# Optimization experiments

Measured on AMD Instinct MI355X. Metric: run time of the kernel, lower is better.

Reference implementation:

```python
import jax, jax.numpy as jnp
import numpy as np

EPS = 1e-05
DELTA = 2.0


def setup_inputs() -> dict:
    key = jax.random.key(0)
    k1, k2, k3, k4 = jax.random.split(key, 4)
    b, n, d = 8, 2048, 256
    static_node_emb = jax.random.normal(k1, (n, d), dtype=jnp.float32)
    current_node_emb = jax.random.normal(k2, (b, n, d), dtype=jnp.float32)
    prev_node_emb = jax.random.normal(k3, (b, n, d), dtype=jnp.float32)
    # xavier_normal for (d, 1): std = sqrt(2/(d+1))
    threshold_pool = jax.random.normal(k4, (d, 1), dtype=jnp.float32) * np.sqrt(2.0 / (d + 1))
    gamma = jnp.ones((1,), dtype=jnp.float32)
    beta = jnp.zeros((1,), dtype=jnp.float32)
    return {
        'static_node_emb': static_node_emb,
        'current_node_emb': current_node_emb,
        'prev_node_emb': prev_node_emb,
        'threshold_pool': threshold_pool,
        'gamma': gamma,
        'beta': beta,
    }


def reference(static_node_emb, current_node_emb, prev_node_emb, threshold_pool, gamma, beta):
    # graph: [b, n, n]
    graph = jnp.einsum('bnd,bmd->bnm', current_node_emb, prev_node_emb)
    # static mask: relu(S S^T) > 0  -> {0,1} float [n, n]
    static_sim = jnp.einsum('nd,md->nm', static_node_emb, static_node_emb)
    static_mask = (jax.nn.relu(static_sim) > 0).astype(jnp.float32)
    # masked relu + row-normalize (asym_adj)
    masked = jax.nn.relu(graph * static_mask) + 1e-10
    probs = masked / jnp.sum(masked, axis=-1, keepdims=True)
    # threshold: sigmoid(cur @ pool) scaled by diagonal of probs
    threshold = jax.nn.sigmoid(jnp.einsum('bnd,dg->bng', current_node_emb, threshold_pool))
    threshold_baseline = jnp.diagonal(probs, axis1=-2, axis2=-1)[..., None]  # [b, n, 1]
    threshold = threshold_baseline * threshold
    x = probs - threshold  # broadcast [b,n,n] - [b,n,1]
    pos_mask = (x >= 0).astype(jnp.float32)
    neg_mask = 1.0 - pos_mask
    pos_mask = jax.nn.sigmoid(x) * pos_mask
    # InstanceNorm over last two dims (biased variance)
    mean = jnp.mean(pos_mask, axis=(-2, -1), keepdims=True)
    var = jnp.var(pos_mask, axis=(-2, -1), keepdims=True)
    x_norm = (pos_mask - mean) / jnp.sqrt(var + EPS)
    tau_beta = jnp.exp((gamma * x_norm + beta) * DELTA)
    phi = tau_beta * pos_mask + tau_beta * neg_mask
    return phi
```

## Files before the change

kernel.cpp:

```cpp
#include <hip/hip_runtime.h>
#include <math.h>
#include <stdint.h>


__device__ __forceinline__ float mrn(float a, float b) { return __fmul_rn(a, b); }
__device__ __forceinline__ float arn(float a, float b) { return __fadd_rn(a, b); }

#define GBK 16

__global__ __launch_bounds__(256)
void mask_kernel(const float* __restrict__ S, unsigned char* __restrict__ mask,
                 int n, int d) {
  __shared__ float Xk[GBK][132];
  __shared__ float Yk[GBK][132];
  const int t = threadIdx.x, tx = t & 15, ty = t >> 4;
  const int row0 = blockIdx.y * 128, col0 = blockIdx.x * 128;
  const int r = t >> 1, q = t & 1;
  float acc[8][8] = {};
  for (int kc = 0; kc < d; kc += GBK) {
    __syncthreads();
    const float* xp = &S[(size_t)(row0 + r) * d + kc + q * 8];
    float4 v0 = *reinterpret_cast<const float4*>(xp);
    float4 v1 = *reinterpret_cast<const float4*>(xp + 4);
    const float* yp = &S[(size_t)(col0 + r) * d + kc + q * 8];
    float4 u0 = *reinterpret_cast<const float4*>(yp);
    float4 u1 = *reinterpret_cast<const float4*>(yp + 4);
    Xk[q*8+0][r] = v0.x; Xk[q*8+1][r] = v0.y; Xk[q*8+2][r] = v0.z; Xk[q*8+3][r] = v0.w;
    Xk[q*8+4][r] = v1.x; Xk[q*8+5][r] = v1.y; Xk[q*8+6][r] = v1.z; Xk[q*8+7][r] = v1.w;
    Yk[q*8+0][r] = u0.x; Yk[q*8+1][r] = u0.y; Yk[q*8+2][r] = u0.z; Yk[q*8+3][r] = u0.w;
    Yk[q*8+4][r] = u1.x; Yk[q*8+5][r] = u1.y; Yk[q*8+6][r] = u1.z; Yk[q*8+7][r] = u1.w;
    __syncthreads();
#pragma unroll
    for (int k = 0; k < GBK; ++k) {
      float4 a0 = *reinterpret_cast<const float4*>(&Xk[k][ty * 8]);
      float4 a1 = *reinterpret_cast<const float4*>(&Xk[k][ty * 8 + 4]);
      float4 b0 = *reinterpret_cast<const float4*>(&Yk[k][tx * 4]);
      float4 b1 = *reinterpret_cast<const float4*>(&Yk[k][64 + tx * 4]);
      float a[8] = {a0.x, a0.y, a0.z, a0.w, a1.x, a1.y, a1.z, a1.w};
      float b[8] = {b0.x, b0.y, b0.z, b0.w, b1.x, b1.y, b1.z, b1.w};
#pragma unroll
      for (int i2 = 0; i2 < 8; ++i2)
#pragma unroll
        for (int j2 = 0; j2 < 8; ++j2)
          acc[i2][j2] = __builtin_fmaf(a[i2], b[j2], acc[i2][j2]);
    }
  }
#pragma unroll
  for (int i2 = 0; i2 < 8; ++i2) {
    int gi = row0 + ty * 8 + i2;
    unsigned lo = 0, hi = 0;
#pragma unroll
    for (int j2 = 0; j2 < 4; ++j2) {
      lo |= (acc[i2][j2]     > 0.0f ? 1u : 0u) << (8 * j2);
      hi |= (acc[i2][4 + j2] > 0.0f ? 1u : 0u) << (8 * j2);
    }
    *reinterpret_cast<unsigned*>(&mask[(size_t)gi * n + col0 + tx * 4])      = lo;
    *reinterpret_cast<unsigned*>(&mask[(size_t)gi * n + col0 + 64 + tx * 4]) = hi;
  }
}

__global__ __launch_bounds__(512)
void graph_kernel(const float* __restrict__ cur_, const float* __restrict__ prev,
                  const unsigned char* __restrict__ mask, float* __restrict__ wout,
                  int n, int d) {
  __shared__ float Xk[GBK][260];
  __shared__ float Yk[GBK][132];
  const int t = threadIdx.x;
  const int tx = t & 15, ty = t >> 4;
  const int row0 = blockIdx.y * 256, col0 = blockIdx.x * 128, bz = blockIdx.z;
  const float* X = cur_ + (size_t)bz * n * d;
  const float* Y = prev + (size_t)bz * n * d;
  const int ra = t >> 1, qa = t & 1;
  const int rb = t >> 2, qb = t & 3;
  float acc[8][8] = {};
  for (int kc = 0; kc < d; kc += GBK) {
    __syncthreads();
    const float* xp = &X[(size_t)(row0 + ra) * d + kc + qa * 8];
    float4 v0 = *reinterpret_cast<const float4*>(xp);
    float4 v1 = *reinterpret_cast<const float4*>(xp + 4);
    const float* yp = &Y[(size_t)(col0 + rb) * d + kc + qb * 4];
    float4 u0 = *reinterpret_cast<const float4*>(yp);
    Xk[qa*8+0][ra] = v0.x; Xk[qa*8+1][ra] = v0.y; Xk[qa*8+2][ra] = v0.z; Xk[qa*8+3][ra] = v0.w;
    Xk[qa*8+4][ra] = v1.x; Xk[qa*8+5][ra] = v1.y; Xk[qa*8+6][ra] = v1.z; Xk[qa*8+7][ra] = v1.w;
    Yk[qb*4+0][rb] = u0.x; Yk[qb*4+1][rb] = u0.y; Yk[qb*4+2][rb] = u0.z; Yk[qb*4+3][rb] = u0.w;
    __syncthreads();
#pragma unroll
    for (int k = 0; k < GBK; ++k) {
      float4 a0 = *reinterpret_cast<const float4*>(&Xk[k][ty * 8]);
      float4 a1 = *reinterpret_cast<const float4*>(&Xk[k][ty * 8 + 4]);
      float4 b0 = *reinterpret_cast<const float4*>(&Yk[k][tx * 4]);
      float4 b1 = *reinterpret_cast<const float4*>(&Yk[k][64 + tx * 4]);
      float a[8] = {a0.x, a0.y, a0.z, a0.w, a1.x, a1.y, a1.z, a1.w};
      float b[8] = {b0.x, b0.y, b0.z, b0.w, b1.x, b1.y, b1.z, b1.w};
#pragma unroll
      for (int i2 = 0; i2 < 8; ++i2)
#pragma unroll
        for (int j2 = 0; j2 < 8; ++j2)
          acc[i2][j2] = __builtin_fmaf(a[i2], b[j2], acc[i2][j2]);
    }
  }
#pragma unroll
  for (int i2 = 0; i2 < 8; ++i2) {
    int gi = row0 + ty * 8 + i2;
    size_t rbase = (size_t)bz * n * n + (size_t)gi * n;
    unsigned mlo = *reinterpret_cast<const unsigned*>(&mask[(size_t)gi * n + col0 + tx * 4]);
    unsigned mhi = *reinterpret_cast<const unsigned*>(&mask[(size_t)gi * n + col0 + 64 + tx * 4]);
    float4 o0, o1;
    o0.x = arn(fmaxf(mrn(acc[i2][0], (float)(mlo & 0xff)), 0.0f), 1e-10f);
    o0.y = arn(fmaxf(mrn(acc[i2][1], (float)((mlo >> 8) & 0xff)), 0.0f), 1e-10f);
    o0.z = arn(fmaxf(mrn(acc[i2][2], (float)((mlo >> 16) & 0xff)), 0.0f), 1e-10f);
    o0.w = arn(fmaxf(mrn(acc[i2][3], (float)((mlo >> 24) & 0xff)), 0.0f), 1e-10f);
    o1.x = arn(fmaxf(mrn(acc[i2][4], (float)(mhi & 0xff)), 0.0f), 1e-10f);
    o1.y = arn(fmaxf(mrn(acc[i2][5], (float)((mhi >> 8) & 0xff)), 0.0f), 1e-10f);
    o1.z = arn(fmaxf(mrn(acc[i2][6], (float)((mhi >> 16) & 0xff)), 0.0f), 1e-10f);
    o1.w = arn(fmaxf(mrn(acc[i2][7], (float)((mhi >> 24) & 0xff)), 0.0f), 1e-10f);
    *reinterpret_cast<float4*>(&wout[rbase + col0 + tx * 4])      = o0;
    *reinterpret_cast<float4*>(&wout[rbase + col0 + 64 + tx * 4]) = o1;
  }
}

__global__ __launch_bounds__(256)
void tz_kernel(const float* __restrict__ cur, const float* __restrict__ pool,
               float* __restrict__ tv, int nrows, int d) {
  int row = blockIdx.x * 256 + threadIdx.x;
  if (row >= nrows) return;
  const float* x = cur + (size_t)row * d;
  float acc = 0.0f;
  for (int k = 0; k < d; ++k) acc = __builtin_fmaf(x[k], pool[k], acc);
  float e = (float)exp(-(double)acc);
  tv[row] = __fdiv_rn(1.0f, arn(1.0f, e));
}

__global__ __launch_bounds__(256)
void rowstat_kernel(const float* __restrict__ wbuf, const float* __restrict__ tv,
                    float* __restrict__ rsv, float* __restrict__ thrv,
                    double* __restrict__ cpart, int n) {
  const int row = blockIdx.x;
  const int t = threadIdx.x;
  const float* a = wbuf + (size_t)row * n;
  const int i = row % n;
  const int kleaf = t >> 4, l = t & 15;
  __shared__ float leaf[16];
  __shared__ float sh_rs, sh_thr;
  {
    const float* base = a + kleaf * 128;
    float r0 = base[l],      r1 = base[16 + l],  r2 = base[32 + l],  r3 = base[48 + l];
    float r4 = base[64 + l], r5 = base[80 + l],  r6 = base[96 + l],  r7 = base[112 + l];
    float v = arn(arn(arn(r0, r1), arn(r2, r3)), arn(arn(r4, r5), arn(r6, r7)));
    v = arn(v, __shfl_xor(v, 8));
    v = arn(v, __shfl_xor(v, 4));
    v = arn(v, __shfl_xor(v, 2));
    v = arn(v, __shfl_xor(v, 1));
    if (l == 0) leaf[kleaf] = v;
  }
  __syncthreads();
  if (t == 0) {
    float t1[8], t2[4], t3[2];
#pragma unroll
    for (int k2 = 0; k2 < 8; ++k2) t1[k2] = arn(leaf[2*k2], leaf[2*k2+1]);
#pragma unroll
    for (int k2 = 0; k2 < 4; ++k2) t2[k2] = arn(t1[2*k2], t1[2*k2+1]);
#pragma unroll
    for (int k2 = 0; k2 < 2; ++k2) t3[k2] = arn(t2[2*k2], t2[2*k2+1]);
    float rs = arn(t3[0], t3[1]);
    float tb = __fdiv_rn(a[i], rs);
    float th = mrn(tb, tv[row]);
    sh_rs = rs; sh_thr = th;
    rsv[row] = rs; thrv[row] = th;
  }
  __syncthreads();
  const float rs = sh_rs, thr = sh_thr;
  double s1 = 0.0, s2 = 0.0;
  for (int off = 0; off < n; off += 1024) {
    float4 wv = *reinterpret_cast<const float4*>(&a[off + t * 4]);
    float wa[4] = {wv.x, wv.y, wv.z, wv.w};
#pragma unroll
    for (int c = 0; c < 4; ++c) {
      float probs = __fdiv_rn(wa[c], rs);
      float x = __fsub_rn(probs, thr);
      if (x >= 0.0f) {
        float pv = __fdiv_rn(1.0f, arn(1.0f, expf(-x)));
        s1 += (double)pv;
        s2 += (double)pv * (double)pv;
      }
    }
  }
  __shared__ double sh1[256], sh2[256];
  sh1[t] = s1; sh2[t] = s2;
  __syncthreads();
  for (int s = 128; s > 0; s >>= 1) {
    if (t < s) { sh1[t] += sh1[t + s]; sh2[t] += sh2[t + s]; }
    __syncthreads();
  }
  if (t == 0) {
    cpart[(size_t)row * 2 + 0] = sh1[0];
    cpart[(size_t)row * 2 + 1] = sh2[0];
  }
}

__global__ __launch_bounds__(256)
void stats_kernel(const double* __restrict__ cpart, float* __restrict__ bstats,
                  int nb, double inv_nn) {
  int b = blockIdx.x, t = threadIdx.x;
  double s1 = 0.0, s2 = 0.0;
  for (int c = t; c < nb; c += 256) {
    s1 += cpart[((size_t)b * nb + c) * 2 + 0];
    s2 += cpart[((size_t)b * nb + c) * 2 + 1];
  }
  __shared__ double sh1[256], sh2[256];
  sh1[t] = s1; sh2[t] = s2;
  __syncthreads();
  for (int s = 128; s > 0; s >>= 1) {
    if (t < s) { sh1[t] += sh1[t + s]; sh2[t] += sh2[t + s]; }
    __syncthreads();
  }
  if (t == 0) {
    double mean = sh1[0] * inv_nn;
    double var = sh2[0] * inv_nn - mean * mean;
    bstats[b * 2 + 0] = (float)mean;
    bstats[b * 2 + 1] = (float)(1.0 / sqrt(var + 1e-5));
  }
}

__global__ __launch_bounds__(256)
void phi_kernel(float4* __restrict__ buf, const float* __restrict__ rsv,
                const float* __restrict__ thrv, const float* __restrict__ bstats,
                const float* __restrict__ gamma, const float* __restrict__ beta,
                size_t total4, int nq, int n) {
  size_t idx = (size_t)blockIdx.x * blockDim.x + threadIdx.x;
  if (idx >= total4) return;
  int row = (int)(idx / (size_t)nq);
  int b = row / n;
  float rs = rsv[row], thr = thrv[row];
  float mean = bstats[b * 2 + 0];
  float inv = bstats[b * 2 + 1];
  float ga = gamma[0] * 2.0f;
  float be = beta[0] * 2.0f;
  float4 v = buf[idx];
  float wa[4] = {v.x, v.y, v.z, v.w};
  float oa[4];
#pragma unroll
  for (int c = 0; c < 4; ++c) {
    float probs = __fdiv_rn(wa[c], rs);
    float x = __fsub_rn(probs, thr);
    float p = 0.0f, m = 1.0f;
    if (x >= 0.0f) {
      p = __fdiv_rn(1.0f, arn(1.0f, expf(-x)));
      m = p;
    }
    float xn = (p - mean) * inv;
    oa[c] = expf(ga * xn + be) * m;
  }
  v.x = oa[0]; v.y = oa[1]; v.z = oa[2]; v.w = oa[3];
  buf[idx] = v;
}

extern "C" void kernel_launch(void* const* d_in, const int* in_sizes, int n_in,
                              void* d_out, int out_size, void* d_ws, size_t ws_size,
                              hipStream_t stream) {
  const float* S     = (const float*)d_in[0];
  const float* cur   = (const float*)d_in[1];
  const float* prev  = (const float*)d_in[2];
  const float* pool  = (const float*)d_in[3];
  const float* gamma = (const float*)d_in[4];
  const float* beta  = (const float*)d_in[5];
  const int d = in_sizes[3];
  const int n = in_sizes[0] / d;
  const int b = in_sizes[1] / (n * d);
  float* out = (float*)d_out;

  const int nrows = b * n;

  char* ws = (char*)d_ws;
  float* tv   = (float*)ws; ws += (size_t)nrows * sizeof(float);
  float* rsv  = (float*)ws; ws += (size_t)nrows * sizeof(float);
  float* thrv = (float*)ws; ws += (size_t)nrows * sizeof(float);
  ws = (char*)(((uintptr_t)ws + 15) & ~(uintptr_t)15);
  double* cpart = (double*)ws; ws += (size_t)nrows * 2 * sizeof(double);
  float* bstats = (float*)ws;  ws += 64;
  unsigned char* mask = (unsigned char*)ws;

  hipLaunchKernelGGL(mask_kernel, dim3(n / 128, n / 128), dim3(256), 0, stream,
                     S, mask, n, d);
  hipLaunchKernelGGL(tz_kernel, dim3((nrows + 255) / 256), dim3(256), 0, stream,
                     cur, pool, tv, nrows, d);
  hipLaunchKernelGGL(graph_kernel, dim3(n / 128, n / 256, b), dim3(512), 0, stream,
                     cur, prev, mask, out, n, d);
  hipLaunchKernelGGL(rowstat_kernel, dim3(nrows), dim3(256), 0, stream,
                     out, tv, rsv, thrv, cpart, n);
  hipLaunchKernelGGL(stats_kernel, dim3(b), dim3(256), 0, stream,
                     cpart, bstats, n, 1.0 / ((double)n * (double)n));
  size_t total4 = (size_t)b * n * n / 4;
  hipLaunchKernelGGL(phi_kernel, dim3((unsigned)((total4 + 255) / 256)), dim3(256), 0, stream,
                     (float4*)out, rsv, thrv, bstats, gamma, beta, total4, n / 4, n);
}
```

Baseline: 373.4 us.

## Double per-thread register tile in graph GEMM and halve block size

The graph GEMM now runs 256 threads per block, each computing a 16x8 output micro-tile instead of 8x8, which raises arithmetic intensity per shared-memory read. Global loads are issued before the first barrier so they can overlap the previous iteration's compute. The cost is a 128-float accumulator array per thread and more register pressure. The launch bounds request 3 blocks per CU, which may force spills or reduce occupancy.

```diff
diff --git a/kernel.cpp b/kernel.cpp
--- a/kernel.cpp
+++ b/kernel.cpp
@@ -59,7 +59,7 @@
   }
 }
 
-__global__ __launch_bounds__(512)
+__global__ __launch_bounds__(256, 3)
 void graph_kernel(const float* __restrict__ cur_, const float* __restrict__ prev,
                   const unsigned char* __restrict__ mask, float* __restrict__ wout,
                   int n, int d) {
@@ -70,38 +70,48 @@
   const int row0 = blockIdx.y * 256, col0 = blockIdx.x * 128, bz = blockIdx.z;
   const float* X = cur_ + (size_t)bz * n * d;
   const float* Y = prev + (size_t)bz * n * d;
-  const int ra = t >> 1, qa = t & 1;
-  const int rb = t >> 2, qb = t & 3;
-  float acc[8][8] = {};
+  const int rbB = t >> 1, qb = t & 1;
+  const float* xbase = &X[(size_t)(row0 + t) * d];
+  const float* ybase = &Y[(size_t)(col0 + rbB) * d + qb * 8];
+  float acc[16][8] = {};
   for (int kc = 0; kc < d; kc += GBK) {
-    __syncthreads();
-    const float* xp = &X[(size_t)(row0 + ra) * d + kc + qa * 8];
-    float4 v0 = *reinterpret_cast<const float4*>(xp);
-    float4 v1 = *reinterpret_cast<const float4*>(xp + 4);
-    const float* yp = &Y[(size_t)(col0 + rb) * d + kc + qb * 4];
-    float4 u0 = *reinterpret_cast<const float4*>(yp);
-    Xk[qa*8+0][ra] = v0.x; Xk[qa*8+1][ra] = v0.y; Xk[qa*8+2][ra] = v0.z; Xk[qa*8+3][ra] = v0.w;
-    Xk[qa*8+4][ra] = v1.x; Xk[qa*8+5][ra] = v1.y; Xk[qa*8+6][ra] = v1.z; Xk[qa*8+7][ra] = v1.w;
-    Yk[qb*4+0][rb] = u0.x; Yk[qb*4+1][rb] = u0.y; Yk[qb*4+2][rb] = u0.z; Yk[qb*4+3][rb] = u0.w;
+    float4 v0 = *reinterpret_cast<const float4*>(xbase + kc);
+    float4 v1 = *reinterpret_cast<const float4*>(xbase + kc + 4);
+    float4 v2 = *reinterpret_cast<const float4*>(xbase + kc + 8);
+    float4 v3 = *reinterpret_cast<const float4*>(xbase + kc + 12);
+    float4 u0 = *reinterpret_cast<const float4*>(ybase + kc);
+    float4 u1 = *reinterpret_cast<const float4*>(ybase + kc + 4);
+    __syncthreads();
+    Xk[ 0][t] = v0.x; Xk[ 1][t] = v0.y; Xk[ 2][t] = v0.z; Xk[ 3][t] = v0.w;
+    Xk[ 4][t] = v1.x; Xk[ 5][t] = v1.y; Xk[ 6][t] = v1.z; Xk[ 7][t] = v1.w;
+    Xk[ 8][t] = v2.x; Xk[ 9][t] = v2.y; Xk[10][t] = v2.z; Xk[11][t] = v2.w;
+    Xk[12][t] = v3.x; Xk[13][t] = v3.y; Xk[14][t] = v3.z; Xk[15][t] = v3.w;
+    Yk[qb*8+0][rbB] = u0.x; Yk[qb*8+1][rbB] = u0.y;
+    Yk[qb*8+2][rbB] = u0.z; Yk[qb*8+3][rbB] = u0.w;
+    Yk[qb*8+4][rbB] = u1.x; Yk[qb*8+5][rbB] = u1.y;
+    Yk[qb*8+6][rbB] = u1.z; Yk[qb*8+7][rbB] = u1.w;
     __syncthreads();
 #pragma unroll
     for (int k = 0; k < GBK; ++k) {
-      float4 a0 = *reinterpret_cast<const float4*>(&Xk[k][ty * 8]);
-      float4 a1 = *reinterpret_cast<const float4*>(&Xk[k][ty * 8 + 4]);
+      float4 a0 = *reinterpret_cast<const float4*>(&Xk[k][ty * 16]);
+      float4 a1 = *reinterpret_cast<const float4*>(&Xk[k][ty * 16 + 4]);
+      float4 a2 = *reinterpret_cast<const float4*>(&Xk[k][ty * 16 + 8]);
+      float4 a3 = *reinterpret_cast<const float4*>(&Xk[k][ty * 16 + 12]);
       float4 b0 = *reinterpret_cast<const float4*>(&Yk[k][tx * 4]);
       float4 b1 = *reinterpret_cast<const float4*>(&Yk[k][64 + tx * 4]);
-      float a[8] = {a0.x, a0.y, a0.z, a0.w, a1.x, a1.y, a1.z, a1.w};
-      float b[8] = {b0.x, b0.y, b0.z, b0.w, b1.x, b1.y, b1.z, b1.w};
-#pragma unroll
-      for (int i2 = 0; i2 < 8; ++i2)
+      float a[16] = {a0.x, a0.y, a0.z, a0.w, a1.x, a1.y, a1.z, a1.w,
+                     a2.x, a2.y, a2.z, a2.w, a3.x, a3.y, a3.z, a3.w};
+      float b[8]  = {b0.x, b0.y, b0.z, b0.w, b1.x, b1.y, b1.z, b1.w};
+#pragma unroll
+      for (int i2 = 0; i2 < 16; ++i2)
 #pragma unroll
         for (int j2 = 0; j2 < 8; ++j2)
           acc[i2][j2] = __builtin_fmaf(a[i2], b[j2], acc[i2][j2]);
     }
   }
 #pragma unroll
-  for (int i2 = 0; i2 < 8; ++i2) {
-    int gi = row0 + ty * 8 + i2;
+  for (int i2 = 0; i2 < 16; ++i2) {
+    int gi = row0 + ty * 16 + i2;
     size_t rbase = (size_t)bz * n * n + (size_t)gi * n;
     unsigned mlo = *reinterpret_cast<const unsigned*>(&mask[(size_t)gi * n + col0 + tx * 4]);
     unsigned mhi = *reinterpret_cast<const unsigned*>(&mask[(size_t)gi * n + col0 + 64 + tx * 4]);
@@ -284,7 +294,7 @@
                      S, mask, n, d);
   hipLaunchKernelGGL(tz_kernel, dim3((nrows + 255) / 256), dim3(256), 0, stream,
                      cur, pool, tv, nrows, d);
-  hipLaunchKernelGGL(graph_kernel, dim3(n / 128, n / 256, b), dim3(512), 0, stream,
+  hipLaunchKernelGGL(graph_kernel, dim3(n / 128, n / 256, b), dim3(256), 0, stream,
                      cur, prev, mask, out, n, d);
   hipLaunchKernelGGL(rowstat_kernel, dim3(nrows), dim3(256), 0, stream,
                      out, tv, rsv, thrv, cpart, n);
```

New measurement: 372.5 us. About the same (-0.3%).
